# Performance work log

Measured on AMD Instinct MI355X. Metric: run time of the kernel, lower is better.

## Reference

```python
import jax, jax.numpy as jnp
import numpy as np

B = 262144
IN = 256
HID = 128
OUT = 15
C = 15  # num_cameras


def setup_inputs() -> dict:
    key = jax.random.key(0)
    k_x, k_c, k_w1, k_b1, k_w2, k_b2 = jax.random.split(key, 6)
    x = jax.random.normal(k_x, (B, IN), dtype=jnp.float32)
    cam = jax.random.randint(k_c, (B,), 0, C)
    # per-camera 2-layer MLP params (Linear->ReLU->Dropout(eval)->Linear)
    W1 = jax.random.normal(k_w1, (C, IN, HID), dtype=jnp.float32) / np.sqrt(IN)
    b1 = jax.random.normal(k_b1, (C, HID), dtype=jnp.float32) * 0.01
    W2 = jax.random.normal(k_w2, (C, HID, OUT), dtype=jnp.float32) / np.sqrt(HID)
    b2 = jax.random.normal(k_b2, (C, OUT), dtype=jnp.float32) * 0.01
    return {"input": x, "cam": cam, "W1": W1, "b1": b1, "W2": W2, "b2": b2}


def reference(input, cam, W1, b1, W2, b2):
    # Per-sample camera-id dispatch to one of C small MLPs, vectorized:
    # run each camera's MLP on the full batch (C is small/fixed) and select
    # each sample's output by its camera id. Dropout is identity (eval mode).
    out = jnp.zeros((input.shape[0], OUT), dtype=input.dtype)
    for c in range(C):
        h = jax.nn.relu(input @ W1[c] + b1[c])      # [B, HID]
        logits = h @ W2[c] + b2[c]                  # [B, OUT]
        out = jnp.where((cam == c)[:, None], logits, out)
    return out
```

## Files before the change

### kernel.cpp

```cpp
#include <hip/hip_runtime.h>
#include <hip/hip_bf16.h>

#define BB    262144
#define INF   256
#define HIDF  128
#define OUTF  15
#define NCAM  15
#define TM    128
#define MAXTILES (BB/TM + NCAM)

typedef __attribute__((ext_vector_type(8))) short          bf16x8;
typedef __attribute__((ext_vector_type(4))) float          floatx4;
typedef __attribute__((ext_vector_type(4))) int            intx4;
typedef __attribute__((ext_vector_type(4))) unsigned int   uintx4;
typedef __attribute__((ext_vector_type(8))) unsigned short ushortx8;

__device__ __forceinline__ unsigned short f2bf1(float a){
  unsigned int u = __builtin_bit_cast(unsigned int, a);
  u += 0x7fffu + ((u >> 16) & 1u);
  return (unsigned short)(u >> 16);
}
__device__ __forceinline__ unsigned int f2bf2(float a, float b){
  return (unsigned int)f2bf1(a) | ((unsigned int)f2bf1(b) << 16);
}

__global__ void k_prephist(const float* __restrict__ W1, const float* __restrict__ W2,
                           const int* __restrict__ cam,
                           unsigned short* __restrict__ W1p, unsigned short* __restrict__ W2p,
                           int* __restrict__ counts){
  int bid = blockIdx.x, tid = threadIdx.x;
  if (bid < 240){
    int t = bid * 256 + tid;
    int l  = t & 63;
    int kf = (t >> 6) & 7;
    int nf = (t >> 9) & 7;
    int c  = t >> 12;
    int col = nf*16 + (l & 15);
    int k0  = kf*32 + (l >> 4)*8;
    ushortx8 v;
    #pragma unroll
    for (int j = 0; j < 8; ++j)
      v[j] = f2bf1(W1[((size_t)c*INF + k0 + j)*HIDF + col]);
    *reinterpret_cast<ushortx8*>(W1p + (size_t)t*8) = v;
  } else if (bid < 255){
    int c  = bid - 240;
    int l  = tid & 63;
    int kf = tid >> 6;
    int col = l & 15;
    int k0  = kf*32 + (l >> 4)*8;
    ushortx8 v;
    #pragma unroll
    for (int j = 0; j < 8; ++j){
      float f = (col < OUTF) ? W2[((size_t)c*HIDF + k0 + j)*OUTF + col] : 0.0f;
      v[j] = f2bf1(f);
    }
    *reinterpret_cast<ushortx8*>(W2p + ((size_t)(c*4 + kf)*64 + l)*8) = v;
  } else if (bid >= 256){
    __shared__ int lc[NCAM];
    if (tid < NCAM) lc[tid] = 0;
    __syncthreads();
    intx4 v = *reinterpret_cast<const intx4*>(cam + (size_t)((bid-256)*256 + tid)*4);
    atomicAdd(&lc[v[0]], 1); atomicAdd(&lc[v[1]], 1);
    atomicAdd(&lc[v[2]], 1); atomicAdd(&lc[v[3]], 1);
    __syncthreads();
    if (tid < NCAM && lc[tid]) atomicAdd(&counts[tid], lc[tid]);
  }
}

__global__ void k_scatter(const int* __restrict__ cam, const int* __restrict__ counts,
                          int* __restrict__ scatterOfs, int* __restrict__ idx){
  __shared__ int lc[NCAM];
  __shared__ int loff[NCAM];
  __shared__ int base[NCAM];
  int t = threadIdx.x;
  if (t < NCAM) lc[t] = 0;
  __syncthreads();
  int start = blockIdx.x * 4096;
  int camr[16], lpos[16];
  #pragma unroll
  for (int j = 0; j < 16; ++j){
    int i = start + j*256 + t;
    camr[j] = cam[i];
    lpos[j] = atomicAdd(&lc[camr[j]], 1);
  }
  __syncthreads();
  if (t == 0){
    int s = 0;
    #pragma unroll
    for (int c = 0; c < NCAM; ++c){ loff[c] = s; s += counts[c]; }
  }
  __syncthreads();
  if (t < NCAM) base[t] = loff[t] + atomicAdd(&scatterOfs[t], lc[t]);
  __syncthreads();
  #pragma unroll
  for (int j = 0; j < 16; ++j)
    idx[base[camr[j]] + lpos[j]] = start + j*256 + t;
}

__global__ __launch_bounds__(256, 2) void k_mlp(
    const float* __restrict__ x, const int* __restrict__ idx,
    const int* __restrict__ counts,
    const unsigned short* __restrict__ W1p, const unsigned short* __restrict__ W2p,
    const float* __restrict__ b1, const float* __restrict__ b2,
    float* __restrict__ out)
{
  __shared__ __align__(16) char smem[65536 + 512];
  int* sidx = reinterpret_cast<int*>(smem + 65536);

  int bid = blockIdx.x;
  int c = -1, segStart = 0, rowStart = 0, rows = 0;
  {
    int cum = 0, rcum = 0;
    #pragma unroll 1
    for (int cc = 0; cc < NCAM; ++cc){
      int n  = counts[cc];
      int nt = (n + TM - 1) / TM;
      if (c < 0 && bid < cum + nt){
        c = cc;
        rowStart = (bid - cum) * TM;
        segStart = rcum;
        rows = n - rowStart; if (rows > TM) rows = TM;
      }
      cum += nt; rcum += n;
    }
  }
  if (c < 0) return;

  int t = threadIdx.x;
  int wave = t >> 6, lane = t & 63;

  {
    const char* gsrc = reinterpret_cast<const char*>(W1p + (size_t)c*32768);
    #pragma unroll
    for (int i = 0; i < 16; ++i){
      int ci = i*4 + wave;
      __builtin_amdgcn_global_load_lds(
        (const __attribute__((address_space(1))) unsigned int*)(gsrc + ci*1024 + lane*16),
        (__attribute__((address_space(3))) unsigned int*)(smem + ci*1024),
        16, 0, 0);
    }
  }
  if (t < TM){
    int r = (t < rows) ? t : (rows - 1);
    sidx[t] = idx[segStart + rowStart + r];
  }
  __syncthreads();

  int wr  = wave * 32;
  int l15 = lane & 15, lk = lane >> 4;

  const float* ap0 = x + (size_t)sidx[wr + l15]      * INF + lk*8;
  const float* ap1 = x + (size_t)sidx[wr + 16 + l15] * INF + lk*8;

  floatx4 acc[2][8];
  #pragma unroll
  for (int i = 0; i < 2; ++i)
    #pragma unroll
    for (int j = 0; j < 8; ++j) acc[i][j] = (floatx4)0.0f;

  floatx4 a[4][4];
  #pragma unroll
  for (int s = 0; s < 4; ++s){
    a[s][0] = *reinterpret_cast<const floatx4*>(ap0 + s*32);
    a[s][1] = *reinterpret_cast<const floatx4*>(ap0 + s*32 + 4);
    a[s][2] = *reinterpret_cast<const floatx4*>(ap1 + s*32);
    a[s][3] = *reinterpret_cast<const floatx4*>(ap1 + s*32 + 4);
  }

  #pragma unroll
  for (int kf = 0; kf < 8; ++kf){
    const int cur = kf & 3;
    bf16x8 bf[8];
    #pragma unroll
    for (int nf = 0; nf < 8; ++nf)
      bf[nf] = *reinterpret_cast<const bf16x8*>(smem + (nf*8 + kf)*1024 + lane*16);
    uintx4 u0, u1;
    u0[0] = f2bf2(a[cur][0][0], a[cur][0][1]); u0[1] = f2bf2(a[cur][0][2], a[cur][0][3]);
    u0[2] = f2bf2(a[cur][1][0], a[cur][1][1]); u0[3] = f2bf2(a[cur][1][2], a[cur][1][3]);
    u1[0] = f2bf2(a[cur][2][0], a[cur][2][1]); u1[1] = f2bf2(a[cur][2][2], a[cur][2][3]);
    u1[2] = f2bf2(a[cur][3][0], a[cur][3][1]); u1[3] = f2bf2(a[cur][3][2], a[cur][3][3]);
    bf16x8 af0 = __builtin_bit_cast(bf16x8, u0);
    bf16x8 af1 = __builtin_bit_cast(bf16x8, u1);
    if (kf < 4){
      a[cur][0] = *reinterpret_cast<const floatx4*>(ap0 + (kf+4)*32);
      a[cur][1] = *reinterpret_cast<const floatx4*>(ap0 + (kf+4)*32 + 4);
      a[cur][2] = *reinterpret_cast<const floatx4*>(ap1 + (kf+4)*32);
      a[cur][3] = *reinterpret_cast<const floatx4*>(ap1 + (kf+4)*32 + 4);
    }
    #pragma unroll
    for (int nf = 0; nf < 8; ++nf)
      acc[0][nf] = __builtin_amdgcn_mfma_f32_16x16x32_bf16(af0, bf[nf], acc[0][nf], 0, 0, 0);
    #pragma unroll
    for (int nf = 0; nf < 8; ++nf)
      acc[1][nf] = __builtin_amdgcn_mfma_f32_16x16x32_bf16(af1, bf[nf], acc[1][nf], 0, 0, 0);
  }

  __syncthreads();

  #pragma unroll
  for (int nf = 0; nf < 8; ++nf){
    int col = nf*16 + l15;
    float bias = b1[c*HIDF + col];
    #pragma unroll
    for (int mf = 0; mf < 2; ++mf){
      #pragma unroll
      for (int j = 0; j < 4; ++j){
        int row = wr + mf*16 + lk*4 + j;
        float h = fmaxf(acc[mf][nf][j] + bias, 0.0f);
        int off = row*256 + ((col*2) ^ ((row & 7) << 4));
        *reinterpret_cast<unsigned short*>(smem + off) = f2bf1(h);
      }
    }
  }
  __syncthreads();

  floatx4 acc2[2];
  acc2[0] = (floatx4)0.0f; acc2[1] = (floatx4)0.0f;
  const unsigned short* wb = W2p + (size_t)c*2048 + lane*8;
  #pragma unroll
  for (int kf = 0; kf < 4; ++kf){
    bf16x8 wv = *reinterpret_cast<const bf16x8*>(wb + kf*512);
    #pragma unroll
    for (int mf = 0; mf < 2; ++mf){
      int row = wr + mf*16 + l15;
      int off = row*256 + ((kf*64 + lk*16) ^ ((row & 7) << 4));
      bf16x8 av = *reinterpret_cast<const bf16x8*>(smem + off);
      acc2[mf] = __builtin_amdgcn_mfma_f32_16x16x32_bf16(av, wv, acc2[mf], 0, 0, 0);
    }
  }

  int col = l15;
  if (col < OUTF){
    float bias2 = b2[c*OUTF + col];
    #pragma unroll
    for (int mf = 0; mf < 2; ++mf){
      #pragma unroll
      for (int j = 0; j < 4; ++j){
        int r = wr + mf*16 + lk*4 + j;
        if (r < rows)
          out[(size_t)sidx[r]*OUTF + col] = acc2[mf][j] + bias2;
      }
    }
  }
}

extern "C" void kernel_launch(void* const* d_in, const int* in_sizes, int n_in,
                              void* d_out, int out_size, void* d_ws, size_t ws_size,
                              hipStream_t stream) {
  const float* x  = (const float*)d_in[0];
  const int*   cam= (const int*)d_in[1];
  const float* W1 = (const float*)d_in[2];
  const float* b1 = (const float*)d_in[3];
  const float* W2 = (const float*)d_in[4];
  const float* b2 = (const float*)d_in[5];
  float* out = (float*)d_out;

  char* ws = (char*)d_ws;
  int* counts     = (int*)(ws);
  int* scatterOfs = (int*)(ws + 64);
  int* idx        = (int*)(ws + 256);
  unsigned short* W1p = (unsigned short*)(ws + 256 + (size_t)BB*4);
  unsigned short* W2p = W1p + (size_t)NCAM*8*8*64*8;

  (void)hipMemsetAsync(counts, 0, 128, stream);
  hipLaunchKernelGGL(k_prephist, dim3(512),     dim3(256), 0, stream, W1, W2, cam, W1p, W2p, counts);
  hipLaunchKernelGGL(k_scatter,  dim3(BB/4096), dim3(256), 0, stream, cam, counts, scatterOfs, idx);
  hipLaunchKernelGGL(k_mlp,      dim3(MAXTILES),dim3(256), 0, stream,
                     x, idx, counts, W1p, W2p, b1, b2, out);
}
```

Baseline: 103.1 us.

## Stage gathered x rows through double-buffered LDS, read W1 from global

The gathered input rows are now copied into LDS with asynchronous global-to-LDS loads, using a swizzled double buffer in 64-column chunks that overlap with the MFMA loop. The W1 fragments are read straight from global memory into a register double buffer instead of being staged in LDS. The goal is to hide gather latency and free LDS for the activation pipeline, at the cost of a barrier per stage and W1 traffic through the cache rather than shared memory. The sidx shared array is dropped and indices are read from global at output time.

```diff
diff --git a/kernel.cpp b/kernel.cpp
--- a/kernel.cpp
+++ b/kernel.cpp
@@ -104,8 +104,7 @@
     const float* __restrict__ b1, const float* __restrict__ b2,
     float* __restrict__ out)
 {
-  __shared__ __align__(16) char smem[65536 + 512];
-  int* sidx = reinterpret_cast<int*>(smem + 65536);
+  __shared__ __align__(16) char smem[65536];
 
   int bid = blockIdx.x;
   int c = -1, segStart = 0, rowStart = 0, rows = 0;
@@ -128,29 +127,36 @@
 
   int t = threadIdx.x;
   int wave = t >> 6, lane = t & 63;
-
-  {
-    const char* gsrc = reinterpret_cast<const char*>(W1p + (size_t)c*32768);
-    #pragma unroll
-    for (int i = 0; i < 16; ++i){
-      int ci = i*4 + wave;
-      __builtin_amdgcn_global_load_lds(
-        (const __attribute__((address_space(1))) unsigned int*)(gsrc + ci*1024 + lane*16),
-        (__attribute__((address_space(3))) unsigned int*)(smem + ci*1024),
-        16, 0, 0);
-    }
-  }
-  if (t < TM){
-    int r = (t < rows) ? t : (rows - 1);
-    sidx[t] = idx[segStart + rowStart + r];
-  }
-  __syncthreads();
-
   int wr  = wave * 32;
   int l15 = lane & 15, lk = lane >> 4;
-
-  const float* ap0 = x + (size_t)sidx[wr + l15]      * INF + lk*8;
-  const float* ap1 = x + (size_t)sidx[wr + 16 + l15] * INF + lk*8;
+  const int* idxBase = idx + segStart + rowStart;
+
+  const char* srcp[8];
+  {
+    int rowsel = lane >> 4;
+    int w = (lane & 15) * 16;
+    #pragma unroll
+    for (int i = 0; i < 8; ++i){
+      int row = wr + i*4 + rowsel;
+      int rc = (row < rows) ? row : (rows - 1);
+      int g = idxBase[rc];
+      int offr = w ^ (((i*4 + rowsel) & 7) << 4);
+      srcp[i] = reinterpret_cast<const char*>(x) + (size_t)g*1024 + offr;
+    }
+  }
+
+  #define STAGE(q) { \
+    char* dbase = smem + ((q)&1)*32768 + wave*8192; \
+    _Pragma("unroll") \
+    for (int i = 0; i < 8; ++i){ \
+      __builtin_amdgcn_global_load_lds( \
+        (const __attribute__((address_space(1))) unsigned int*)(srcp[i] + (q)*256), \
+        (__attribute__((address_space(3))) unsigned int*)(dbase + i*1024), \
+        16, 0, 0); \
+    } \
+  }
+
+  const unsigned short* bbase = W1p + (size_t)c*32768 + lane*8;
 
   floatx4 acc[2][8];
   #pragma unroll
@@ -158,44 +164,49 @@
     #pragma unroll
     for (int j = 0; j < 8; ++j) acc[i][j] = (floatx4)0.0f;
 
-  floatx4 a[4][4];
-  #pragma unroll
-  for (int s = 0; s < 4; ++s){
-    a[s][0] = *reinterpret_cast<const floatx4*>(ap0 + s*32);
-    a[s][1] = *reinterpret_cast<const floatx4*>(ap0 + s*32 + 4);
-    a[s][2] = *reinterpret_cast<const floatx4*>(ap1 + s*32);
-    a[s][3] = *reinterpret_cast<const floatx4*>(ap1 + s*32 + 4);
-  }
-
-  #pragma unroll
-  for (int kf = 0; kf < 8; ++kf){
-    const int cur = kf & 3;
-    bf16x8 bf[8];
-    #pragma unroll
-    for (int nf = 0; nf < 8; ++nf)
-      bf[nf] = *reinterpret_cast<const bf16x8*>(smem + (nf*8 + kf)*1024 + lane*16);
-    uintx4 u0, u1;
-    u0[0] = f2bf2(a[cur][0][0], a[cur][0][1]); u0[1] = f2bf2(a[cur][0][2], a[cur][0][3]);
-    u0[2] = f2bf2(a[cur][1][0], a[cur][1][1]); u0[3] = f2bf2(a[cur][1][2], a[cur][1][3]);
-    u1[0] = f2bf2(a[cur][2][0], a[cur][2][1]); u1[1] = f2bf2(a[cur][2][2], a[cur][2][3]);
-    u1[2] = f2bf2(a[cur][3][0], a[cur][3][1]); u1[3] = f2bf2(a[cur][3][2], a[cur][3][3]);
-    bf16x8 af0 = __builtin_bit_cast(bf16x8, u0);
-    bf16x8 af1 = __builtin_bit_cast(bf16x8, u1);
-    if (kf < 4){
-      a[cur][0] = *reinterpret_cast<const floatx4*>(ap0 + (kf+4)*32);
-      a[cur][1] = *reinterpret_cast<const floatx4*>(ap0 + (kf+4)*32 + 4);
-      a[cur][2] = *reinterpret_cast<const floatx4*>(ap1 + (kf+4)*32);
-      a[cur][3] = *reinterpret_cast<const floatx4*>(ap1 + (kf+4)*32 + 4);
-    }
-    #pragma unroll
-    for (int nf = 0; nf < 8; ++nf)
-      acc[0][nf] = __builtin_amdgcn_mfma_f32_16x16x32_bf16(af0, bf[nf], acc[0][nf], 0, 0, 0);
-    #pragma unroll
-    for (int nf = 0; nf < 8; ++nf)
-      acc[1][nf] = __builtin_amdgcn_mfma_f32_16x16x32_bf16(af1, bf[nf], acc[1][nf], 0, 0, 0);
-  }
-
-  __syncthreads();
+  bf16x8 bfr[2][8];
+
+  STAGE(0);
+  #pragma unroll
+  for (int nf = 0; nf < 8; ++nf)
+    bfr[0][nf] = *reinterpret_cast<const bf16x8*>(bbase + nf*4096);
+  __syncthreads();
+
+  int swz = (l15 & 7) << 4;
+
+  #pragma unroll
+  for (int q = 0; q < 4; ++q){
+    if (q < 3) STAGE(q+1);
+    #pragma unroll
+    for (int kfl = 0; kfl < 2; ++kfl){
+      const int kf = q*2 + kfl;
+      if (kf < 7){
+        #pragma unroll
+        for (int nf = 0; nf < 8; ++nf)
+          bfr[(kf+1)&1][nf] = *reinterpret_cast<const bf16x8*>(bbase + nf*4096 + (kf+1)*512);
+      }
+      bf16x8 af[2];
+      #pragma unroll
+      for (int mf = 0; mf < 2; ++mf){
+        int row = wr + mf*16 + l15;
+        const char* rbase = smem + (q&1)*32768 + row*256;
+        int w1 = kfl*128 + lk*32;
+        floatx4 f0 = *reinterpret_cast<const floatx4*>(rbase + (w1 ^ swz));
+        floatx4 f1 = *reinterpret_cast<const floatx4*>(rbase + ((w1+16) ^ swz));
+        uintx4 u;
+        u[0] = f2bf2(f0[0], f0[1]); u[1] = f2bf2(f0[2], f0[3]);
+        u[2] = f2bf2(f1[0], f1[1]); u[3] = f2bf2(f1[2], f1[3]);
+        af[mf] = __builtin_bit_cast(bf16x8, u);
+      }
+      #pragma unroll
+      for (int nf = 0; nf < 8; ++nf)
+        acc[0][nf] = __builtin_amdgcn_mfma_f32_16x16x32_bf16(af[0], bfr[kf&1][nf], acc[0][nf], 0, 0, 0);
+      #pragma unroll
+      for (int nf = 0; nf < 8; ++nf)
+        acc[1][nf] = __builtin_amdgcn_mfma_f32_16x16x32_bf16(af[1], bfr[kf&1][nf], acc[1][nf], 0, 0, 0);
+    }
+    __syncthreads();
+  }
 
   #pragma unroll
   for (int nf = 0; nf < 8; ++nf){
@@ -238,10 +249,11 @@
       for (int j = 0; j < 4; ++j){
         int r = wr + mf*16 + lk*4 + j;
         if (r < rows)
-          out[(size_t)sidx[r]*OUTF + col] = acc2[mf][j] + bias2;
-      }
-    }
-  }
+          out[(size_t)idxBase[r]*OUTF + col] = acc2[mf][j] + bias2;
+      }
+    }
+  }
+  #undef STAGE
 }
 
 extern "C" void kernel_launch(void* const* d_in, const int* in_sizes, int n_in,
```

After: 95.52 us. 1.08x faster.

## Stream activation rows into LDS via async global_load_lds ring buffer

Applied to the files above, without the earlier changes.

Replaces the per-lane register prefetch of gathered fp32 input rows with asynchronous global-to-LDS copies into a 4-slot swizzled ring buffer per wave, paced by explicit vmcnt waits. The hidden activations are written into per-wave regions of that buffer, which removes two block-wide barriers. LDS use doubles to 128KB and launch bounds drop to one block per CU. The goal is deeper memory-level parallelism on the gathered x loads, at the cost of occupancy.

```diff
diff --git a/kernel.cpp b/kernel.cpp
--- a/kernel.cpp
+++ b/kernel.cpp
@@ -97,15 +97,16 @@
     idx[base[camr[j]] + lpos[j]] = start + j*256 + t;
 }
 
-__global__ __launch_bounds__(256, 2) void k_mlp(
+__global__ __launch_bounds__(256, 1) void k_mlp(
     const float* __restrict__ x, const int* __restrict__ idx,
     const int* __restrict__ counts,
     const unsigned short* __restrict__ W1p, const unsigned short* __restrict__ W2p,
     const float* __restrict__ b1, const float* __restrict__ b2,
     float* __restrict__ out)
 {
-  __shared__ __align__(16) char smem[65536 + 512];
-  int* sidx = reinterpret_cast<int*>(smem + 65536);
+  __shared__ __align__(16) char smem[131072 + 512];
+  int* sidx = reinterpret_cast<int*>(smem + 131072);
+  char* Ab = smem + 65536;
 
   int bid = blockIdx.x;
   int c = -1, segStart = 0, rowStart = 0, rows = 0;
@@ -149,8 +150,28 @@
   int wr  = wave * 32;
   int l15 = lane & 15, lk = lane >> 4;
 
-  const float* ap0 = x + (size_t)sidx[wr + l15]      * INF + lk*8;
-  const float* ap1 = x + (size_t)sidx[wr + 16 + l15] * INF + lk*8;
+  const char* srcp[4];
+  {
+    int sr = lane >> 3, w = lane & 7;
+    int woff = (w ^ sr) * 16;
+    #pragma unroll
+    for (int i = 0; i < 4; ++i){
+      int row = wr + i*8 + sr;
+      int rc = (row < rows) ? row : (rows - 1);
+      srcp[i] = reinterpret_cast<const char*>(x) + (size_t)sidx[rc]*1024 + woff;
+    }
+  }
+
+  #define STAGE(q) { \
+    char* db = Ab + ((q)&3)*16384 + wave*4096; \
+    _Pragma("unroll") \
+    for (int i = 0; i < 4; ++i){ \
+      __builtin_amdgcn_global_load_lds( \
+        (const __attribute__((address_space(1))) unsigned int*)(srcp[i] + (q)*128), \
+        (__attribute__((address_space(3))) unsigned int*)(db + i*1024), \
+        16, 0, 0); \
+    } \
+  }
 
   floatx4 acc[2][8];
   #pragma unroll
@@ -158,44 +179,42 @@
     #pragma unroll
     for (int j = 0; j < 8; ++j) acc[i][j] = (floatx4)0.0f;
 
-  floatx4 a[4][4];
-  #pragma unroll
-  for (int s = 0; s < 4; ++s){
-    a[s][0] = *reinterpret_cast<const floatx4*>(ap0 + s*32);
-    a[s][1] = *reinterpret_cast<const floatx4*>(ap0 + s*32 + 4);
-    a[s][2] = *reinterpret_cast<const floatx4*>(ap1 + s*32);
-    a[s][3] = *reinterpret_cast<const floatx4*>(ap1 + s*32 + 4);
-  }
+  STAGE(0); STAGE(1); STAGE(2);
+
+  int swz8 = l15 & 7;
 
   #pragma unroll
   for (int kf = 0; kf < 8; ++kf){
-    const int cur = kf & 3;
+    if (kf < 5) STAGE(kf+3);
+    if (kf < 5)       asm volatile("s_waitcnt vmcnt(12)" ::: "memory");
+    else if (kf == 5) asm volatile("s_waitcnt vmcnt(8)"  ::: "memory");
+    else if (kf == 6) asm volatile("s_waitcnt vmcnt(4)"  ::: "memory");
+    else              asm volatile("s_waitcnt vmcnt(0)"  ::: "memory");
+
     bf16x8 bf[8];
     #pragma unroll
     for (int nf = 0; nf < 8; ++nf)
-      bf[nf] = *reinterpret_cast<const bf16x8*>(smem + (nf*8 + kf)*1024 + lane*16);
-    uintx4 u0, u1;
-    u0[0] = f2bf2(a[cur][0][0], a[cur][0][1]); u0[1] = f2bf2(a[cur][0][2], a[cur][0][3]);
-    u0[2] = f2bf2(a[cur][1][0], a[cur][1][1]); u0[3] = f2bf2(a[cur][1][2], a[cur][1][3]);
-    u1[0] = f2bf2(a[cur][2][0], a[cur][2][1]); u1[1] = f2bf2(a[cur][2][2], a[cur][2][3]);
-    u1[2] = f2bf2(a[cur][3][0], a[cur][3][1]); u1[3] = f2bf2(a[cur][3][2], a[cur][3][3]);
-    bf16x8 af0 = __builtin_bit_cast(bf16x8, u0);
-    bf16x8 af1 = __builtin_bit_cast(bf16x8, u1);
-    if (kf < 4){
-      a[cur][0] = *reinterpret_cast<const floatx4*>(ap0 + (kf+4)*32);
-      a[cur][1] = *reinterpret_cast<const floatx4*>(ap0 + (kf+4)*32 + 4);
-      a[cur][2] = *reinterpret_cast<const floatx4*>(ap1 + (kf+4)*32);
-      a[cur][3] = *reinterpret_cast<const floatx4*>(ap1 + (kf+4)*32 + 4);
+      bf[nf] = *reinterpret_cast<const bf16x8*>(smem + (size_t)(nf*8 + kf)*1024 + lane*16);
+
+    bf16x8 af[2];
+    #pragma unroll
+    for (int mf = 0; mf < 2; ++mf){
+      int rl = mf*16 + l15;
+      const char* rb = Ab + (kf&3)*16384 + wave*4096 + rl*128;
+      floatx4 f0 = *reinterpret_cast<const floatx4*>(rb + (((lk*2)   ^ swz8) * 16));
+      floatx4 f1 = *reinterpret_cast<const floatx4*>(rb + (((lk*2+1) ^ swz8) * 16));
+      uintx4 u;
+      u[0] = f2bf2(f0[0], f0[1]); u[1] = f2bf2(f0[2], f0[3]);
+      u[2] = f2bf2(f1[0], f1[1]); u[3] = f2bf2(f1[2], f1[3]);
+      af[mf] = __builtin_bit_cast(bf16x8, u);
     }
     #pragma unroll
     for (int nf = 0; nf < 8; ++nf)
-      acc[0][nf] = __builtin_amdgcn_mfma_f32_16x16x32_bf16(af0, bf[nf], acc[0][nf], 0, 0, 0);
+      acc[0][nf] = __builtin_amdgcn_mfma_f32_16x16x32_bf16(af[0], bf[nf], acc[0][nf], 0, 0, 0);
     #pragma unroll
     for (int nf = 0; nf < 8; ++nf)
-      acc[1][nf] = __builtin_amdgcn_mfma_f32_16x16x32_bf16(af1, bf[nf], acc[1][nf], 0, 0, 0);
-  }
-
-  __syncthreads();
+      acc[1][nf] = __builtin_amdgcn_mfma_f32_16x16x32_bf16(af[1], bf[nf], acc[1][nf], 0, 0, 0);
+  }
 
   #pragma unroll
   for (int nf = 0; nf < 8; ++nf){
@@ -205,14 +224,13 @@
     for (int mf = 0; mf < 2; ++mf){
       #pragma unroll
       for (int j = 0; j < 4; ++j){
-        int row = wr + mf*16 + lk*4 + j;
+        int rl = mf*16 + lk*4 + j;
         float h = fmaxf(acc[mf][nf][j] + bias, 0.0f);
-        int off = row*256 + ((col*2) ^ ((row & 7) << 4));
-        *reinterpret_cast<unsigned short*>(smem + off) = f2bf1(h);
+        int off = (rl>>4)*16384 + wave*4096 + (rl&15)*256 + ((col*2) ^ ((rl&7)<<4));
+        *reinterpret_cast<unsigned short*>(Ab + off) = f2bf1(h);
       }
     }
   }
-  __syncthreads();
 
   floatx4 acc2[2];
   acc2[0] = (floatx4)0.0f; acc2[1] = (floatx4)0.0f;
@@ -222,9 +240,9 @@
     bf16x8 wv = *reinterpret_cast<const bf16x8*>(wb + kf*512);
     #pragma unroll
     for (int mf = 0; mf < 2; ++mf){
-      int row = wr + mf*16 + l15;
-      int off = row*256 + ((kf*64 + lk*16) ^ ((row & 7) << 4));
-      bf16x8 av = *reinterpret_cast<const bf16x8*>(smem + off);
+      int rl = mf*16 + l15;
+      int off = (rl>>4)*16384 + wave*4096 + (rl&15)*256 + ((kf*64 + lk*16) ^ ((rl&7)<<4));
+      bf16x8 av = *reinterpret_cast<const bf16x8*>(Ab + off);
       acc2[mf] = __builtin_amdgcn_mfma_f32_16x16x32_bf16(av, wv, acc2[mf], 0, 0, 0);
     }
   }
@@ -242,6 +260,7 @@
       }
     }
   }
+  #undef STAGE
 }
 
 extern "C" void kernel_launch(void* const* d_in, const int* in_sizes, int n_in,
```

Measured after the change: 107.3 us. 1.04x slower.
